# Kernel optimization log

Measured on AMD Instinct MI355X. Metric: run time of the kernel, lower is better.

Reference implementation:

```python
import jax, jax.numpy as jnp
import numpy as np

N_NODES = 12000
N_EDGES = 384000
F_IN = 128       # num_features
D = 64           # latent_dim (hidden_dim), num_gc_layers = 1
H_DEC = 64       # ceil(F_IN / 2)
BN_EPS = 1e-4


def _gcn_conv(x, W, b, src, dst, n):
    # PyG GCNConv: h = x @ W; add self-loops; sym-normalized scatter-add; + bias
    h = x @ W
    loop = jnp.arange(n)
    s = jnp.concatenate([src, loop])
    d = jnp.concatenate([dst, loop])
    deg = jax.ops.segment_sum(jnp.ones(s.shape[0], dtype=x.dtype), d, num_segments=n)
    dis = jax.lax.rsqrt(deg)  # deg >= 1 thanks to self-loops
    norm = dis[s] * dis[d]    # [E+N]
    out = jax.ops.segment_sum(h[s] * norm[:, None], d, num_segments=n)
    return out + b


def _bn_train(x, gamma, beta):
    # BatchNorm1d, training-mode batch statistics, biased variance, eps=1e-4
    mu = jnp.mean(x, axis=0)
    xc = x - mu
    var = jnp.mean(xc * xc, axis=0)
    return xc * jax.lax.rsqrt(var + BN_EPS) * gamma + beta


def _enc_layer(x, W, b, g, be, src, dst, n):
    # GCNConv -> Sigmoid -> (dropout no-op) -> BatchNorm
    return _bn_train(jax.nn.sigmoid(_gcn_conv(x, W, b, src, dst, n)), g, be)


def setup_inputs() -> dict:
    key = jax.random.key(0)
    ks = jax.random.split(key, 16)
    inp = {
        'x': jax.random.normal(ks[0], (N_NODES, F_IN), dtype=jnp.float32),
        'src': jax.random.randint(ks[1], (N_EDGES,), 0, N_NODES),
        'dst': jax.random.randint(ks[2], (N_EDGES,), 0, N_NODES),
        'batch': jnp.zeros((N_NODES,), dtype=jnp.int32),
        'noise': jax.random.normal(ks[3], (N_NODES, D), dtype=jnp.float32),
        # base_gcn encoder (GCNConv F_IN -> D, BN)
        'W0': jax.random.normal(ks[4], (F_IN, D), dtype=jnp.float32) * 0.08,
        'b0': jnp.zeros((D,), dtype=jnp.float32),
        'g0': jnp.ones((D,), dtype=jnp.float32),
        'be0': jnp.zeros((D,), dtype=jnp.float32),
        # gcn_mean encoder (GCNConv D -> D, BN)
        'Wm': jax.random.normal(ks[5], (D, D), dtype=jnp.float32) * 0.12,
        'bm': jnp.zeros((D,), dtype=jnp.float32),
        'gm': jnp.ones((D,), dtype=jnp.float32),
        'bem': jnp.zeros((D,), dtype=jnp.float32),
        # gcn_logstddev encoder (GCNConv D -> D, BN)
        'Ws': jax.random.normal(ks[6], (D, D), dtype=jnp.float32) * 0.12,
        'bs': jnp.zeros((D,), dtype=jnp.float32),
        'gs': jnp.ones((D,), dtype=jnp.float32),
        'bes': jnp.zeros((D,), dtype=jnp.float32),
        # decoder MLP: Linear(D, H_DEC) -> LeakyReLU -> Linear(H_DEC, F_IN)
        'Dw1': jax.random.normal(ks[7], (D, H_DEC), dtype=jnp.float32) * 0.12,
        'Db1': jnp.zeros((H_DEC,), dtype=jnp.float32),
        'Dw2': jax.random.normal(ks[8], (H_DEC, F_IN), dtype=jnp.float32) * 0.12,
        'Db2': jnp.zeros((F_IN,), dtype=jnp.float32),
    }
    return inp


def reference(x, src, dst, batch, noise,
              W0, b0, g0, be0,
              Wm, bm, gm, bem,
              Ws, bs, gs, bes,
              Dw1, Db1, Dw2, Db2):
    n = x.shape[0]
    hidden = _enc_layer(x, W0, b0, g0, be0, src, dst, n)          # [N, D]
    mean = _enc_layer(hidden, Wm, bm, gm, bem, src, dst, n)       # [N, D]
    logstd = _enc_layer(hidden, Ws, bs, gs, bes, src, dst, n)     # [N, D]
    z = noise * jnp.exp(logstd) + mean                            # reparam trick
    # decoder MLP (LeakyReLU default slope 0.01)
    h = jax.nn.leaky_relu(z @ Dw1 + Db1, negative_slope=0.01)
    reconstructed_x = h @ Dw2 + Db2                               # [N, F_IN]
    A_pred = jax.nn.sigmoid(z @ z.T)                              # [N, N]
    return (reconstructed_x, A_pred)
```

## Files before the change

kernel.cpp:

```cpp
#include <hip/hip_runtime.h>
#include <hip/hip_bf16.h>

#define N_NODES 12000
#define N_EDGES 384000
#define F_INN   128
#define DLAT    64
#define BN_EPS  1e-4f

__device__ __forceinline__ float sigmoidf(float x) { return 1.0f / (1.0f + __expf(-x)); }

__global__ void k_init(int* cnt, int* cur, int n) {
    int i = blockIdx.x * blockDim.x + threadIdx.x;
    if (i < n) { cnt[i] = 0; cur[i] = 0; }
}

__global__ void k_count(const int* dst, int* cnt, int e) {
    int i = blockIdx.x * blockDim.x + threadIdx.x;
    if (i < e) atomicAdd(&cnt[dst[i]], 1);
}

__global__ void k_scan(const int* __restrict__ cnt, int* __restrict__ offs,
                       float* __restrict__ dis, int n) {
    __shared__ int wsum[16];
    int tid = threadIdx.x;
    int base = tid * 12;
    int v[12];
    int s = 0;
#pragma unroll
    for (int q = 0; q < 12; q++) {
        int i = base + q;
        v[q] = (i < n) ? cnt[i] : 0;
        s += v[q];
        if (i < n) dis[i] = rsqrtf((float)(v[q] + 1));
    }
    int lane = tid & 63, w = tid >> 6;
    int ps = s;
#pragma unroll
    for (int o = 1; o < 64; o <<= 1) {
        int t2 = __shfl_up(ps, o, 64);
        if (lane >= o) ps += t2;
    }
    if (lane == 63) wsum[w] = ps;
    __syncthreads();
    if (tid == 0) {
        int acc = 0;
        for (int i = 0; i < 16; i++) { int t2 = wsum[i]; wsum[i] = acc; acc += t2; }
    }
    __syncthreads();
    int acc = wsum[w] + ps - s;
#pragma unroll
    for (int q = 0; q < 12; q++) {
        int i = base + q;
        if (i < n) offs[i] = acc;
        acc += v[q];
        if (i == n - 1) offs[n] = acc;
    }
}

__global__ void k_scatter(const int* src, const int* dst, const int* offs, int* cur,
                          int* ssrc, int e) {
    int i = blockIdx.x * blockDim.x + threadIdx.x;
    if (i < e) {
        int d = dst[i];
        int p = atomicAdd(&cur[d], 1);
        ssrc[offs[d] + p] = src[i];
    }
}

__global__ void k_mm(const float* __restrict__ X, int n, int K,
                     const float* __restrict__ Wa, int Ma,
                     const float* __restrict__ Wb, int Mb,
                     float* __restrict__ out) {
    __shared__ float Wl[8192];
    int M = Ma + Mb;
    for (int idx = threadIdx.x; idx < K * M; idx += blockDim.x) {
        int k = idx / M, m = idx % M;
        Wl[idx] = (m < Ma) ? Wa[k * Ma + m] : Wb[k * Mb + (m - Ma)];
    }
    __syncthreads();
    int rpb = blockDim.x / M;
    int r = blockIdx.x * rpb + threadIdx.x / M;
    int m = threadIdx.x % M;
    if (r >= n) return;
    const float* xr = X + (size_t)r * K;
    float acc = 0.f;
    for (int k = 0; k < K; k++) acc += xr[k] * Wl[k * M + m];
    out[(size_t)r * M + m] = acc;
}

__global__ void k_agg(const float* __restrict__ h, const float* __restrict__ dis,
                      const int* __restrict__ offs, const int* __restrict__ ssrc,
                      const float* __restrict__ ba, const float* __restrict__ bb, int Ma,
                      float* __restrict__ out, int dim, int n) {
    int t = blockIdx.x * blockDim.x + threadIdx.x;
    int node = t / dim;
    if (node >= n) return;
    int f = t - node * dim;
    float di = dis[node];
    float acc = h[(size_t)node * dim + f] * di;
    int e0 = offs[node], e1 = offs[node + 1];
    int j = e0;
    for (; j + 3 < e1; j += 4) {
        int s0 = ssrc[j], s1 = ssrc[j + 1], s2 = ssrc[j + 2], s3 = ssrc[j + 3];
        acc += h[(size_t)s0 * dim + f] * dis[s0];
        acc += h[(size_t)s1 * dim + f] * dis[s1];
        acc += h[(size_t)s2 * dim + f] * dis[s2];
        acc += h[(size_t)s3 * dim + f] * dis[s3];
    }
    for (; j < e1; j++) {
        int s = ssrc[j];
        acc += h[(size_t)s * dim + f] * dis[s];
    }
    float bias = (f < Ma) ? ba[f] : bb[f - Ma];
    out[(size_t)node * dim + f] = sigmoidf(acc * di + bias);
}

#define STATS_BLOCKS 64
__global__ void k_stats1(const float* __restrict__ act, int dim, int n,
                         float* __restrict__ part) {
    int rpb = 256 / dim;
    int c = threadIdx.x % dim;
    int rloc = threadIdx.x / dim;
    float s = 0.f, s2 = 0.f;
    for (int r = blockIdx.x * rpb + rloc; r < n; r += STATS_BLOCKS * rpb) {
        float v = act[(size_t)r * dim + c];
        s += v; s2 += v * v;
    }
    __shared__ float sh[512];
    sh[threadIdx.x] = s; sh[256 + threadIdx.x] = s2;
    __syncthreads();
    if (rloc == 0) {
        for (int q = 1; q < rpb; q++) {
            s += sh[q * dim + c];
            s2 += sh[256 + q * dim + c];
        }
        part[(size_t)(blockIdx.x * dim + c) * 2] = s;
        part[(size_t)(blockIdx.x * dim + c) * 2 + 1] = s2;
    }
}

__global__ void k_stats2(const float* __restrict__ part, int dim, int n,
                         float* __restrict__ mu, float* __restrict__ var) {
    int c = threadIdx.x;
    if (c >= dim) return;
    float s = 0.f, s2 = 0.f;
    for (int q = 0; q < STATS_BLOCKS; q++) {
        s += part[(size_t)(q * dim + c) * 2];
        s2 += part[(size_t)(q * dim + c) * 2 + 1];
    }
    float m = s / n;
    mu[c] = m;
    var[c] = s2 / n - m * m;
}

__global__ void k_bnapply(const float* __restrict__ in, float* __restrict__ out,
                          const float* __restrict__ mu, const float* __restrict__ var,
                          const float* __restrict__ g, const float* __restrict__ be,
                          int dim, size_t total) {
    size_t i = (size_t)blockIdx.x * blockDim.x + threadIdx.x;
    if (i >= total) return;
    int f = (int)(i % dim);
    out[i] = (in[i] - mu[f]) * rsqrtf(var[f] + BN_EPS) * g[f] + be[f];
}

__global__ void k_z(const float* __restrict__ act2, const float* __restrict__ noise,
                    const float* __restrict__ mu, const float* __restrict__ var,
                    const float* __restrict__ gm, const float* __restrict__ bem,
                    const float* __restrict__ gs, const float* __restrict__ bes,
                    float* __restrict__ z, int n) {
    int i = blockIdx.x * blockDim.x + threadIdx.x;
    if (i >= n * DLAT) return;
    int row = i >> 6, j = i & 63;
    const float* ar = act2 + (size_t)row * 128;
    float m  = (ar[j]      - mu[j])      * rsqrtf(var[j]      + BN_EPS) * gm[j] + bem[j];
    float ls = (ar[j + 64] - mu[j + 64]) * rsqrtf(var[j + 64] + BN_EPS) * gs[j] + bes[j];
    z[i] = noise[i] * __expf(ls) + m;
}

__global__ void k_dec(const float* __restrict__ z,
                      const float* __restrict__ W1, const float* __restrict__ B1,
                      const float* __restrict__ W2, const float* __restrict__ B2,
                      float* __restrict__ out, int n) {
    __shared__ float w1[64 * 64];
    __shared__ float w2[64 * 128];
    __shared__ float zl[16 * 64];
    __shared__ float hl[16 * 64];
    int t = threadIdx.x;
    int row0 = blockIdx.x * 16;
    {
        const float4* W14 = (const float4*)W1;
        const float4* W24 = (const float4*)W2;
        for (int i = t; i < 1024; i += 256) ((float4*)w1)[i] = W14[i];
        for (int i = t; i < 2048; i += 256) ((float4*)w2)[i] = W24[i];
        ((float4*)zl)[t] = ((const float4*)(z + (size_t)row0 * 64))[t];
    }
    __syncthreads();
    {
        int hc = t & 63, rg = t >> 6;
        float a0 = B1[hc], a1 = a0, a2 = a0, a3 = a0;
        int rb = rg * 4;
        for (int k = 0; k < 64; k++) {
            float wv = w1[k * 64 + hc];
            a0 += zl[(rb + 0) * 64 + k] * wv;
            a1 += zl[(rb + 1) * 64 + k] * wv;
            a2 += zl[(rb + 2) * 64 + k] * wv;
            a3 += zl[(rb + 3) * 64 + k] * wv;
        }
        hl[(rb + 0) * 64 + hc] = a0 > 0.f ? a0 : 0.01f * a0;
        hl[(rb + 1) * 64 + hc] = a1 > 0.f ? a1 : 0.01f * a1;
        hl[(rb + 2) * 64 + hc] = a2 > 0.f ? a2 : 0.01f * a2;
        hl[(rb + 3) * 64 + hc] = a3 > 0.f ? a3 : 0.01f * a3;
    }
    __syncthreads();
    {
        int oc = t & 127, rg = t >> 7;
        float o[8];
#pragma unroll
        for (int i = 0; i < 8; i++) o[i] = B2[oc];
        int rb = rg * 8;
        for (int k = 0; k < 64; k++) {
            float wv = w2[k * 128 + oc];
#pragma unroll
            for (int i = 0; i < 8; i++) o[i] += hl[(rb + i) * 64 + k] * wv;
        }
#pragma unroll
        for (int i = 0; i < 8; i++)
            out[(size_t)(row0 + rb + i) * 128 + oc] = o[i];
    }
}

#define TN2 94
__global__ __launch_bounds__(256, 2) void k_apred(const float* __restrict__ z,
                                                  float* __restrict__ out, int n) {
    __shared__ float zi[64 * 128];
    __shared__ float zj[64 * 128];
    int b = blockIdx.x;
    float ff = (float)(2 * TN2 + 1);
    int bi = (int)((ff - sqrtf(ff * ff - 8.0f * (float)b)) * 0.5f);
    while (bi > 0 && b < bi * TN2 - bi * (bi - 1) / 2) bi--;
    while (b >= (bi + 1) * TN2 - (bi + 1) * bi / 2) bi++;
    int bj = bi + (b - (bi * TN2 - bi * (bi - 1) / 2));
    int i0 = bi * 128, j0 = bj * 128;

    int t = threadIdx.x;
    int r = t >> 1, half = t & 1;
    {
        int row = i0 + r;
        const float4* s4 = (const float4*)(z + (size_t)row * 64 + half * 32);
#pragma unroll
        for (int q = 0; q < 8; q++) {
            float4 v = (row < n) ? s4[q] : make_float4(0.f, 0.f, 0.f, 0.f);
            int k = half * 32 + q * 4;
            zi[(k + 0) * 128 + r] = v.x;
            zi[(k + 1) * 128 + r] = v.y;
            zi[(k + 2) * 128 + r] = v.z;
            zi[(k + 3) * 128 + r] = v.w;
        }
        row = j0 + r;
        const float4* s4b = (const float4*)(z + (size_t)row * 64 + half * 32);
#pragma unroll
        for (int q = 0; q < 8; q++) {
            float4 v = (row < n) ? s4b[q] : make_float4(0.f, 0.f, 0.f, 0.f);
            int k = half * 32 + q * 4;
            zj[(k + 0) * 128 + r] = v.x;
            zj[(k + 1) * 128 + r] = v.y;
            zj[(k + 2) * 128 + r] = v.z;
            zj[(k + 3) * 128 + r] = v.w;
        }
    }
    __syncthreads();

    int tx = t & 15, ty = t >> 4;
    int c0 = tx * 8, r0 = ty * 8;
    float acc[8][8] = {};
    for (int k = 0; k < 64; k++) {
        float4 a0 = *(const float4*)&zi[k * 128 + r0];
        float4 a1 = *(const float4*)&zi[k * 128 + r0 + 4];
        float4 b0 = *(const float4*)&zj[k * 128 + c0];
        float4 b1 = *(const float4*)&zj[k * 128 + c0 + 4];
        float av[8] = {a0.x, a0.y, a0.z, a0.w, a1.x, a1.y, a1.z, a1.w};
        float bv[8] = {b0.x, b0.y, b0.z, b0.w, b1.x, b1.y, b1.z, b1.w};
#pragma unroll
        for (int i = 0; i < 8; i++)
#pragma unroll
            for (int j = 0; j < 8; j++) acc[i][j] += av[i] * bv[j];
    }
#pragma unroll
    for (int i = 0; i < 8; i++)
#pragma unroll
        for (int j = 0; j < 8; j++) acc[i][j] = sigmoidf(acc[i][j]);

#pragma unroll
    for (int i = 0; i < 8; i++) {
        int row = i0 + r0 + i;
        if (row >= n) continue;
        if (j0 + c0 + 4 <= n)
            *(float4*)&out[(size_t)row * n + j0 + c0] =
                make_float4(acc[i][0], acc[i][1], acc[i][2], acc[i][3]);
        if (j0 + c0 + 8 <= n)
            *(float4*)&out[(size_t)row * n + j0 + c0 + 4] =
                make_float4(acc[i][4], acc[i][5], acc[i][6], acc[i][7]);
    }
    if (bi != bj) {
#pragma unroll
        for (int j = 0; j < 8; j++) {
            int row = j0 + c0 + j;
            if (row >= n) continue;
            if (i0 + r0 + 4 <= n)
                *(float4*)&out[(size_t)row * n + i0 + r0] =
                    make_float4(acc[0][j], acc[1][j], acc[2][j], acc[3][j]);
            if (i0 + r0 + 8 <= n)
                *(float4*)&out[(size_t)row * n + i0 + r0 + 4] =
                    make_float4(acc[4][j], acc[5][j], acc[6][j], acc[7][j]);
        }
    }
}

extern "C" void kernel_launch(void* const* d_in, const int* in_sizes, int n_in,
                              void* d_out, int out_size, void* d_ws, size_t ws_size,
                              hipStream_t stream) {
    const float* x     = (const float*)d_in[0];
    const int*   src   = (const int*)d_in[1];
    const int*   dst   = (const int*)d_in[2];
    const float* noise = (const float*)d_in[4];
    const float* W0  = (const float*)d_in[5];
    const float* b0  = (const float*)d_in[6];
    const float* g0  = (const float*)d_in[7];
    const float* be0 = (const float*)d_in[8];
    const float* Wm  = (const float*)d_in[9];
    const float* bm  = (const float*)d_in[10];
    const float* gm  = (const float*)d_in[11];
    const float* bem = (const float*)d_in[12];
    const float* Ws  = (const float*)d_in[13];
    const float* bs  = (const float*)d_in[14];
    const float* gs  = (const float*)d_in[15];
    const float* bes = (const float*)d_in[16];
    const float* Dw1 = (const float*)d_in[17];
    const float* Db1 = (const float*)d_in[18];
    const float* Dw2 = (const float*)d_in[19];
    const float* Db2 = (const float*)d_in[20];
    float* out = (float*)d_out;

    const int n = N_NODES, e = N_EDGES;

    int*   cnt  = (int*)d_ws;
    int*   offs = (int*)d_ws + 12032;
    int*   cur  = (int*)d_ws + 24064;
    int*   ssrc = (int*)d_ws + 36096;
    float* dis  = (float*)d_ws + 420096;
    float* mu   = (float*)d_ws + 432128;
    float* var  = (float*)d_ws + 432384;
    float* part = (float*)d_ws + 432640;
    float* bufA = (float*)d_ws + 449024;
    float* bufB = bufA + (size_t)N_NODES * 128;
    float* zbuf = bufB;

    k_init<<<(n + 255) / 256, 256, 0, stream>>>(cnt, cur, n);
    k_count<<<(e + 255) / 256, 256, 0, stream>>>(dst, cnt, e);
    k_scan<<<1, 1024, 0, stream>>>(cnt, offs, dis, n);
    k_scatter<<<(e + 255) / 256, 256, 0, stream>>>(src, dst, offs, cur, ssrc, e);

    k_mm<<<n / 4, 256, 0, stream>>>(x, n, F_INN, W0, DLAT, nullptr, 0, bufA);
    k_agg<<<(n * DLAT) / 256, 256, 0, stream>>>(bufA, dis, offs, ssrc, b0, nullptr, DLAT,
                                                bufB, DLAT, n);
    k_stats1<<<STATS_BLOCKS, 256, 0, stream>>>(bufB, DLAT, n, part);
    k_stats2<<<1, 64, 0, stream>>>(part, DLAT, n, mu, var);
    k_bnapply<<<(n * DLAT) / 256, 256, 0, stream>>>(bufB, bufA, mu, var, g0, be0, DLAT,
                                                    (size_t)n * DLAT);

    k_mm<<<n / 2, 256, 0, stream>>>(bufA, n, DLAT, Wm, DLAT, Ws, DLAT, bufB);
    k_agg<<<(n * 128) / 256, 256, 0, stream>>>(bufB, dis, offs, ssrc, bm, bs, DLAT,
                                               bufA, 128, n);
    k_stats1<<<STATS_BLOCKS, 256, 0, stream>>>(bufA, 128, n, part);
    k_stats2<<<1, 128, 0, stream>>>(part, 128, n, mu, var);

    k_z<<<(n * DLAT) / 256, 256, 0, stream>>>(bufA, noise, mu, var, gm, bem, gs, bes,
                                              zbuf, n);

    k_dec<<<n / 16, 256, 0, stream>>>(zbuf, Dw1, Db1, Dw2, Db2, out, n);

    k_apred<<<TN2 * (TN2 + 1) / 2, 256, 0, stream>>>(zbuf, out + (size_t)n * F_INN, n);
}
```

Before: 1.012 ms.

## Compute A_pred with split-bf16 MFMA instead of FP32 FMA tiles

Converts z into bf16 high and low parts in k_z and computes z·zᵀ tiles with three bf16 MFMA products per fragment to approximate fp32 accuracy. Operands are loaded directly from global memory without LDS staging. This is meant to cut FMA compute in the dense N×N kernel, but the output stores change from float4 vectors to scalar writes, with a poorly coalesced transposed store, which may raise memory traffic cost.

```diff
diff --git a/kernel.cpp b/kernel.cpp
--- a/kernel.cpp
+++ b/kernel.cpp
@@ -7,7 +7,19 @@
 #define DLAT    64
 #define BN_EPS  1e-4f
 
+typedef __attribute__((ext_vector_type(8))) short bf16x8;
+typedef __attribute__((ext_vector_type(4))) float f32x4;
+
 __device__ __forceinline__ float sigmoidf(float x) { return 1.0f / (1.0f + __expf(-x)); }
+
+__device__ __forceinline__ unsigned short f2bf_rne(float x) {
+    unsigned u = __float_as_uint(x);
+    unsigned r = (u + 0x7fffu + ((u >> 16) & 1u)) >> 16;
+    return (unsigned short)r;
+}
+__device__ __forceinline__ float bf2f(unsigned short h) {
+    return __uint_as_float((unsigned)h << 16);
+}
 
 __global__ void k_init(int* cnt, int* cur, int n) {
     int i = blockIdx.x * blockDim.x + threadIdx.x;
@@ -167,14 +179,20 @@
                     const float* __restrict__ mu, const float* __restrict__ var,
                     const float* __restrict__ gm, const float* __restrict__ bem,
                     const float* __restrict__ gs, const float* __restrict__ bes,
-                    float* __restrict__ z, int n) {
+                    float* __restrict__ z, unsigned short* __restrict__ zh,
+                    unsigned short* __restrict__ zl, int n) {
     int i = blockIdx.x * blockDim.x + threadIdx.x;
-    if (i >= n * DLAT) return;
+    if (i >= 12032 * 64) return;
     int row = i >> 6, j = i & 63;
+    if (row >= n) { zh[i] = 0; zl[i] = 0; return; }
     const float* ar = act2 + (size_t)row * 128;
     float m  = (ar[j]      - mu[j])      * rsqrtf(var[j]      + BN_EPS) * gm[j] + bem[j];
     float ls = (ar[j + 64] - mu[j + 64]) * rsqrtf(var[j + 64] + BN_EPS) * gs[j] + bes[j];
-    z[i] = noise[i] * __expf(ls) + m;
+    float zv = noise[i] * __expf(ls) + m;
+    z[i] = zv;
+    unsigned short h = f2bf_rne(zv);
+    zh[i] = h;
+    zl[i] = f2bf_rne(zv - bf2f(h));
 }
 
 __global__ void k_dec(const float* __restrict__ z,
@@ -230,10 +248,9 @@
 }
 
 #define TN2 94
-__global__ __launch_bounds__(256, 2) void k_apred(const float* __restrict__ z,
-                                                  float* __restrict__ out, int n) {
-    __shared__ float zi[64 * 128];
-    __shared__ float zj[64 * 128];
+__global__ __launch_bounds__(256) void k_apred(const unsigned short* __restrict__ zh,
+                                               const unsigned short* __restrict__ zl,
+                                               float* __restrict__ out, int n) {
     int b = blockIdx.x;
     float ff = (float)(2 * TN2 + 1);
     int bi = (int)((ff - sqrtf(ff * ff - 8.0f * (float)b)) * 0.5f);
@@ -243,75 +260,78 @@
     int i0 = bi * 128, j0 = bj * 128;
 
     int t = threadIdx.x;
-    int r = t >> 1, half = t & 1;
-    {
-        int row = i0 + r;
-        const float4* s4 = (const float4*)(z + (size_t)row * 64 + half * 32);
-#pragma unroll
-        for (int q = 0; q < 8; q++) {
-            float4 v = (row < n) ? s4[q] : make_float4(0.f, 0.f, 0.f, 0.f);
-            int k = half * 32 + q * 4;
-            zi[(k + 0) * 128 + r] = v.x;
-            zi[(k + 1) * 128 + r] = v.y;
-            zi[(k + 2) * 128 + r] = v.z;
-            zi[(k + 3) * 128 + r] = v.w;
-        }
-        row = j0 + r;
-        const float4* s4b = (const float4*)(z + (size_t)row * 64 + half * 32);
-#pragma unroll
-        for (int q = 0; q < 8; q++) {
-            float4 v = (row < n) ? s4b[q] : make_float4(0.f, 0.f, 0.f, 0.f);
-            int k = half * 32 + q * 4;
-            zj[(k + 0) * 128 + r] = v.x;
-            zj[(k + 1) * 128 + r] = v.y;
-            zj[(k + 2) * 128 + r] = v.z;
-            zj[(k + 3) * 128 + r] = v.w;
-        }
-    }
-    __syncthreads();
-
-    int tx = t & 15, ty = t >> 4;
-    int c0 = tx * 8, r0 = ty * 8;
-    float acc[8][8] = {};
-    for (int k = 0; k < 64; k++) {
-        float4 a0 = *(const float4*)&zi[k * 128 + r0];
-        float4 a1 = *(const float4*)&zi[k * 128 + r0 + 4];
-        float4 b0 = *(const float4*)&zj[k * 128 + c0];
-        float4 b1 = *(const float4*)&zj[k * 128 + c0 + 4];
-        float av[8] = {a0.x, a0.y, a0.z, a0.w, a1.x, a1.y, a1.z, a1.w};
-        float bv[8] = {b0.x, b0.y, b0.z, b0.w, b1.x, b1.y, b1.z, b1.w};
-#pragma unroll
-        for (int i = 0; i < 8; i++)
-#pragma unroll
-            for (int j = 0; j < 8; j++) acc[i][j] += av[i] * bv[j];
-    }
-#pragma unroll
-    for (int i = 0; i < 8; i++)
-#pragma unroll
-        for (int j = 0; j < 8; j++) acc[i][j] = sigmoidf(acc[i][j]);
-
-#pragma unroll
-    for (int i = 0; i < 8; i++) {
-        int row = i0 + r0 + i;
-        if (row >= n) continue;
-        if (j0 + c0 + 4 <= n)
-            *(float4*)&out[(size_t)row * n + j0 + c0] =
-                make_float4(acc[i][0], acc[i][1], acc[i][2], acc[i][3]);
-        if (j0 + c0 + 8 <= n)
-            *(float4*)&out[(size_t)row * n + j0 + c0 + 4] =
-                make_float4(acc[i][4], acc[i][5], acc[i][6], acc[i][7]);
+    int wave = t >> 6, lane = t & 63;
+    int wr = wave >> 1, wc = wave & 1;
+    int lrow = lane & 15;
+    int kg   = lane >> 4;
+
+    int arow0 = i0 + wr * 64;
+    int brow0 = j0 + wc * 64;
+
+    f32x4 acc[4][4] = {};
+
+#pragma unroll
+    for (int kc = 0; kc < 2; kc++) {
+        int koff = kc * 32 + kg * 8;
+        bf16x8 ah[4], al[4], bh[4], bl[4];
+#pragma unroll
+        for (int f = 0; f < 4; f++) {
+            size_t aoff = (size_t)(arow0 + f * 16 + lrow) * 64 + koff;
+            ah[f] = *(const bf16x8*)(zh + aoff);
+            al[f] = *(const bf16x8*)(zl + aoff);
+            size_t boff = (size_t)(brow0 + f * 16 + lrow) * 64 + koff;
+            bh[f] = *(const bf16x8*)(zh + boff);
+            bl[f] = *(const bf16x8*)(zl + boff);
+        }
+#pragma unroll
+        for (int fi = 0; fi < 4; fi++)
+#pragma unroll
+            for (int fj = 0; fj < 4; fj++) {
+                acc[fi][fj] = __builtin_amdgcn_mfma_f32_16x16x32_bf16(
+                    ah[fi], bh[fj], acc[fi][fj], 0, 0, 0);
+                acc[fi][fj] = __builtin_amdgcn_mfma_f32_16x16x32_bf16(
+                    ah[fi], bl[fj], acc[fi][fj], 0, 0, 0);
+                acc[fi][fj] = __builtin_amdgcn_mfma_f32_16x16x32_bf16(
+                    al[fi], bh[fj], acc[fi][fj], 0, 0, 0);
+            }
+    }
+
+#pragma unroll
+    for (int fi = 0; fi < 4; fi++)
+#pragma unroll
+        for (int fj = 0; fj < 4; fj++)
+#pragma unroll
+            for (int q = 0; q < 4; q++)
+                acc[fi][fj][q] = sigmoidf(acc[fi][fj][q]);
+
+#pragma unroll
+    for (int fi = 0; fi < 4; fi++) {
+#pragma unroll
+        for (int q = 0; q < 4; q++) {
+            int r = arow0 + fi * 16 + kg * 4 + q;
+            if (r < n) {
+#pragma unroll
+                for (int fj = 0; fj < 4; fj++) {
+                    int c = brow0 + fj * 16 + lrow;
+                    if (c < n) out[(size_t)r * n + c] = acc[fi][fj][q];
+                }
+            }
+        }
     }
     if (bi != bj) {
 #pragma unroll
-        for (int j = 0; j < 8; j++) {
-            int row = j0 + c0 + j;
-            if (row >= n) continue;
-            if (i0 + r0 + 4 <= n)
-                *(float4*)&out[(size_t)row * n + i0 + r0] =
-                    make_float4(acc[0][j], acc[1][j], acc[2][j], acc[3][j]);
-            if (i0 + r0 + 8 <= n)
-                *(float4*)&out[(size_t)row * n + i0 + r0 + 4] =
-                    make_float4(acc[4][j], acc[5][j], acc[6][j], acc[7][j]);
+        for (int fj = 0; fj < 4; fj++) {
+            int c = brow0 + fj * 16 + lrow;
+            if (c < n) {
+#pragma unroll
+                for (int fi = 0; fi < 4; fi++) {
+#pragma unroll
+                    for (int q = 0; q < 4; q++) {
+                        int r = arow0 + fi * 16 + kg * 4 + q;
+                        if (r < n) out[(size_t)c * n + r] = acc[fi][fj][q];
+                    }
+                }
+            }
         }
     }
 }
@@ -354,6 +374,8 @@
     float* bufA = (float*)d_ws + 449024;
     float* bufB = bufA + (size_t)N_NODES * 128;
     float* zbuf = bufB;
+    unsigned short* zhbuf = (unsigned short*)((float*)d_ws + 3521024);
+    unsigned short* zlbuf = (unsigned short*)((float*)d_ws + 3906048);
 
     k_init<<<(n + 255) / 256, 256, 0, stream>>>(cnt, cur, n);
     k_count<<<(e + 255) / 256, 256, 0, stream>>>(dst, cnt, e);
@@ -374,10 +396,11 @@
     k_stats1<<<STATS_BLOCKS, 256, 0, stream>>>(bufA, 128, n, part);
     k_stats2<<<1, 128, 0, stream>>>(part, 128, n, mu, var);
 
-    k_z<<<(n * DLAT) / 256, 256, 0, stream>>>(bufA, noise, mu, var, gm, bem, gs, bes,
-                                              zbuf, n);
+    k_z<<<(12032 * 64) / 256, 256, 0, stream>>>(bufA, noise, mu, var, gm, bem, gs, bes,
+                                                zbuf, zhbuf, zlbuf, n);
 
     k_dec<<<n / 16, 256, 0, stream>>>(zbuf, Dw1, Db1, Dw2, Db2, out, n);
 
-    k_apred<<<TN2 * (TN2 + 1) / 2, 256, 0, stream>>>(zbuf, out + (size_t)n * F_INN, n);
-}
+    k_apred<<<TN2 * (TN2 + 1) / 2, 256, 0, stream>>>(zhbuf, zlbuf,
+                                                     out + (size_t)n * F_INN, n);
+}
```

Result: slower. 1.048 ms (+3.5%).
